# Kernel tuning notes

Hardware: AMD Instinct MI355X
Metric: run time of the kernel (lower is better)

The kernel has to match this reference:

```python
import jax, jax.numpy as jnp
import numpy as np

V = 100000
E = 1600000
IN_CH = 128
HEADS = 4
OUT_CH = 16
NEG_SLOPE = 0.2


def setup_inputs() -> dict:
    key = jax.random.key(0)
    k1, k2, k3, k4, k5 = jax.random.split(key, 5)
    x = jax.random.normal(k1, (V, IN_CH), dtype=jnp.float32)
    edge_index = jax.random.randint(k2, (2, E), 0, V, dtype=jnp.int32)
    # Xavier-ish scaled params
    W = jax.random.normal(k3, (IN_CH, HEADS * OUT_CH), dtype=jnp.float32) / np.sqrt(IN_CH)
    a_src = jax.random.normal(k4, (HEADS, OUT_CH), dtype=jnp.float32) / np.sqrt(OUT_CH)
    a_dst = jax.random.normal(k5, (HEADS, OUT_CH), dtype=jnp.float32) / np.sqrt(OUT_CH)
    return {"x": x, "edge_index": edge_index, "W": W, "a_src": a_src, "a_dst": a_dst}


def reference(x, edge_index, W, a_src, a_dst):
    v = x.shape[0]
    h, cout = a_src.shape
    z = (x @ W).reshape(v, h, cout)                      # [V,H,C]
    src, dst = edge_index[0], edge_index[1]
    # per-node attention logits, then gather at edges (same math as gather-then-dot)
    e_src = jnp.einsum("vhc,hc->vh", z, a_src)           # [V,H]
    e_dst = jnp.einsum("vhc,hc->vh", z, a_dst)           # [V,H]
    e = jax.nn.leaky_relu(e_src[src] + e_dst[dst], NEG_SLOPE)  # [E,H]
    # scatter softmax over dst per head
    m = jax.ops.segment_max(e, dst, num_segments=v)      # [V,H]
    # nodes with no incoming edges get -inf max; edges never reference them
    exp_e = jnp.exp(e - m[dst])                          # [E,H]
    denom = jax.ops.segment_sum(exp_e, dst, num_segments=v)  # [V,H]
    alpha = exp_e / (denom[dst] + 1e-9)                  # [E,H]
    # scatter aggregation of weighted source features
    agg = jax.ops.segment_sum(z[src] * alpha[:, :, None], dst, num_segments=v)  # [V,H,C]
    out = jax.nn.elu(agg)
    return out.reshape(v, h * cout)
```

## Files before the change

kernel.cpp:

```cpp
#include <hip/hip_runtime.h>
#include <hip/hip_bf16.h>
#include <cstdint>

#define NV 100000
#define NE 1600000
#define KIN 128
#define NH 4
#define NC 16
#define NF 64
#define NBKT 391
#define BCAP 4608
#define EPW 16
#define BINWG 391
#define GEMMWG 1563
#define XSTR 136

typedef __attribute__((ext_vector_type(8))) short bf16x8;
typedef __attribute__((ext_vector_type(4))) float f32x4;

__device__ __forceinline__ short f2bf(float f) {
    unsigned u = __float_as_uint(f);
    return (short)((u + 0x7FFFu + ((u >> 16) & 1u)) >> 16);
}

__global__ __launch_bounds__(256) void k_prep(
    const float* __restrict__ W, short* __restrict__ wfrag)
{
    const int t = threadIdx.x;
#pragma unroll
    for (int it = 0; it < 4; ++it) {
        const int idx = it * 256 + t;
        const int lane = idx & 63;
        const int ctks = idx >> 6;
        const int ct = ctks >> 2, ks = ctks & 3;
        const int n = lane & 15, quad = lane >> 4;
        short* dst = wfrag + (size_t)idx * 8;
#pragma unroll
        for (int j = 0; j < 8; ++j) {
            const int k = ks * 32 + quad * 8 + j;
            dst[j] = f2bf(W[k * NF + ct * 16 + n]);
        }
    }
}

__global__ __launch_bounds__(256) void k_front(
    const float* __restrict__ x, const short* __restrict__ wfrag,
    const float* __restrict__ a_src, const float* __restrict__ a_dst,
    __hip_bfloat16* __restrict__ z, float* __restrict__ esrc,
    float* __restrict__ edst,
    const int* __restrict__ ei, int* __restrict__ gcur,
    unsigned* __restrict__ barr)
{
    if (blockIdx.x < BINWG) {
        __shared__ int hist[NBKT];
        __shared__ int base[NBKT];
        const int t = threadIdx.x;
        const int e0 = blockIdx.x * (256 * EPW);

        for (int i = t; i < NBKT; i += 256) hist[i] = 0;
        __syncthreads();

        unsigned pk[EPW];
        short bk[EPW];
#pragma unroll
        for (int i = 0; i < EPW; ++i) {
            const int e = e0 + i * 256 + t;
            if (e < NE) {
                const int s = ei[e];
                const int d = ei[NE + e];
                const int b = d >> 8;
                bk[i] = (short)b;
                pk[i] = ((unsigned)(d & 255) << 17) | (unsigned)s;
                atomicAdd(&hist[b], 1);
            } else {
                bk[i] = -1;
            }
        }
        __syncthreads();
        for (int i = t; i < NBKT; i += 256) {
            const int c = hist[i];
            base[i] = c ? atomicAdd(&gcur[i], c) : 0;
            hist[i] = 0;
        }
        __syncthreads();
#pragma unroll
        for (int i = 0; i < EPW; ++i) {
            if (bk[i] >= 0) {
                const int b = bk[i];
                const int pos = base[b] + atomicAdd(&hist[b], 1);
                barr[(size_t)b * BCAP + pos] = pk[i];
            }
        }
    } else {
        __shared__ short xs[64 * XSTR];
        const int t = threadIdx.x;
        const int bb = blockIdx.x - BINWG;
        const float4* __restrict__ x4 = (const float4*)x;

#pragma unroll
        for (int i = 0; i < 8; ++i) {
            const int li = i * 256 + t;
            const int idx = bb * 2048 + li;
            float4 v = make_float4(0.f, 0.f, 0.f, 0.f);
            if (idx < NV * (KIN / 4)) v = x4[idx];
            short* p = &xs[(li >> 5) * XSTR + (li & 31) * 4];
            p[0] = f2bf(v.x); p[1] = f2bf(v.y);
            p[2] = f2bf(v.z); p[3] = f2bf(v.w);
        }
        __syncthreads();

        const int wv = t >> 6;
        const int lane = t & 63;
        const int n = lane & 15;
        const int quad = lane >> 4;

        bf16x8 bf[16];
        const bf16x8* __restrict__ wf = (const bf16x8*)wfrag;
#pragma unroll
        for (int i = 0; i < 16; ++i) bf[i] = wf[i * 64 + lane];

        const short* __restrict__ arow = &xs[(wv * 16 + n) * XSTR];
        f32x4 acc[4];
#pragma unroll
        for (int ct = 0; ct < 4; ++ct) acc[ct] = (f32x4){0.f, 0.f, 0.f, 0.f};

#pragma unroll
        for (int ks = 0; ks < 4; ++ks) {
            const bf16x8 af = *(const bf16x8*)(arow + ks * 32 + quad * 8);
#pragma unroll
            for (int ct = 0; ct < 4; ++ct)
                acc[ct] = __builtin_amdgcn_mfma_f32_16x16x32_bf16(
                    af, bf[ct * 4 + ks], acc[ct], 0, 0, 0);
        }

        float as[4], ad[4];
#pragma unroll
        for (int ct = 0; ct < 4; ++ct) {
            as[ct] = a_src[ct * 16 + n];
            ad[ct] = a_dst[ct * 16 + n];
        }
        unsigned short* __restrict__ zz = (unsigned short*)z;
#pragma unroll
        for (int ct = 0; ct < 4; ++ct) {
#pragma unroll
            for (int reg = 0; reg < 4; ++reg) {
                const int r_g = bb * 64 + wv * 16 + quad * 4 + reg;
                const float v = acc[ct][reg];
                float ps = v * as[ct];
                float pd = v * ad[ct];
#pragma unroll
                for (int m = 8; m >= 1; m >>= 1) {
                    ps += __shfl_xor(ps, m, 16);
                    pd += __shfl_xor(pd, m, 16);
                }
                if (r_g < NV) {
                    zz[(size_t)r_g * NF + ct * 16 + n] = (unsigned short)f2bf(v);
                    if (n == 0) {
                        esrc[r_g * NH + ct] = ps;
                        edst[r_g * NH + ct] = pd;
                    }
                }
            }
        }
    }
}

__global__ __launch_bounds__(512) void k_csr(
    const int* __restrict__ gcur, unsigned* __restrict__ barr,
    int* __restrict__ row, int* __restrict__ deg)
{
    __shared__ unsigned arr[BCAP];
    __shared__ int hist[256];
    __shared__ int off[256];
    const int t = threadIdx.x;
    const int b = blockIdx.x;
    const int f = gcur[b];
    unsigned* __restrict__ bp = barr + (size_t)b * BCAP;

    for (int i = t; i < f; i += 512) arr[i] = bp[i];
    if (t < 256) hist[t] = 0;
    __syncthreads();
    for (int i = t; i < f; i += 512) atomicAdd(&hist[arr[i] >> 17], 1);
    __syncthreads();
    if (t < 256) off[t] = hist[t];
    __syncthreads();
    for (int s = 1; s < 256; s <<= 1) {
        const int v = (t < 256 && t >= s) ? off[t - s] : 0;
        __syncthreads();
        if (t < 256) off[t] += v;
        __syncthreads();
    }
    if (t < 256) {
        const int excl = off[t] - hist[t];
        const int d = b * 256 + t;
        if (d < NV) {
            row[d] = b * BCAP + excl;
            deg[d] = hist[t];
        }
        off[t] = excl;
        hist[t] = 0;
    }
    __syncthreads();
    for (int i = t; i < f; i += 512) {
        const unsigned p = arr[i];
        const int dl = p >> 17;
        const int slot = off[dl] + atomicAdd(&hist[dl], 1);
        bp[slot] = p & 0x1FFFFu;
    }
}

__global__ __launch_bounds__(256) void k_agg(
    const int* __restrict__ row, const int* __restrict__ deg,
    const unsigned* __restrict__ col,
    const float* __restrict__ esrc, const float* __restrict__ edst,
    const __hip_bfloat16* __restrict__ z, float* __restrict__ out)
{
    __shared__ unsigned lsw[4][64][8];
    const int wv = threadIdx.x >> 6;
    const int lane = threadIdx.x & 63;
    const int quad = lane >> 4;
    const int li = lane & 15;
    const int h = li >> 2;
    const int d = (blockIdx.x * 256 + threadIdx.x) >> 6;
    const int begin = row[d];
    const int nd = deg[d];
    const float4 edv = *(const float4*)(edst + d * 4);
    const unsigned short* __restrict__ z16 = (const unsigned short*)z;

    float a0 = 0.f, a1 = 0.f, a2 = 0.f, a3 = 0.f, den = 0.f;
    for (int base = 0; base < nd; base += 64) {
        const int n = min(64, nd - base);
        unsigned sL = 0;
        float4 w4 = make_float4(0.f, 0.f, 0.f, 0.f);
        if (lane < n) {
            sL = col[begin + base + lane];
            const float4 e4 = *(const float4*)(esrc + sL * 4);
            float ev;
            ev = e4.x + edv.x; ev = ev > 0.f ? ev : 0.2f * ev; w4.x = __expf(ev);
            ev = e4.y + edv.y; ev = ev > 0.f ? ev : 0.2f * ev; w4.y = __expf(ev);
            ev = e4.z + edv.z; ev = ev > 0.f ? ev : 0.2f * ev; w4.z = __expf(ev);
            ev = e4.w + edv.w; ev = ev > 0.f ? ev : 0.2f * ev; w4.w = __expf(ev);
        }
        uint4 st0, st1;
        st0.x = sL; st0.y = __float_as_uint(w4.x);
        st0.z = sL; st0.w = __float_as_uint(w4.y);
        st1.x = sL; st1.y = __float_as_uint(w4.z);
        st1.z = sL; st1.w = __float_as_uint(w4.w);
        *(uint4*)&lsw[wv][lane][0] = st0;
        *(uint4*)&lsw[wv][lane][4] = st1;
#pragma unroll 4
        for (int j = 0; j < n; j += 4) {
            const uint2 sw = *(const uint2*)&lsw[wv][j + quad][h * 2];
            const float w = __uint_as_float(sw.y);
            const uint2 zv = *(const uint2*)(z16 + (((size_t)sw.x << 4) + li) * 4);
            a0 = fmaf(w, __uint_as_float(zv.x << 16), a0);
            a1 = fmaf(w, __uint_as_float(zv.x & 0xFFFF0000u), a1);
            a2 = fmaf(w, __uint_as_float(zv.y << 16), a2);
            a3 = fmaf(w, __uint_as_float(zv.y & 0xFFFF0000u), a3);
            den += w;
        }
    }
    a0 += __shfl_xor(a0, 16); a0 += __shfl_xor(a0, 32);
    a1 += __shfl_xor(a1, 16); a1 += __shfl_xor(a1, 32);
    a2 += __shfl_xor(a2, 16); a2 += __shfl_xor(a2, 32);
    a3 += __shfl_xor(a3, 16); a3 += __shfl_xor(a3, 32);
    den += __shfl_xor(den, 16); den += __shfl_xor(den, 32);
    if (lane < 16) {
        const float id = 1.f / (den + 1e-9f);
        float v0 = a0 * id, v1 = a1 * id, v2 = a2 * id, v3 = a3 * id;
        v0 = v0 > 0.f ? v0 : expm1f(v0);
        v1 = v1 > 0.f ? v1 : expm1f(v1);
        v2 = v2 > 0.f ? v2 : expm1f(v2);
        v3 = v3 > 0.f ? v3 : expm1f(v3);
        *(float4*)(out + (size_t)d * NF + li * 4) = make_float4(v0, v1, v2, v3);
    }
}

extern "C" void kernel_launch(void* const* d_in, const int* in_sizes, int n_in,
                              void* d_out, int out_size, void* d_ws, size_t ws_size,
                              hipStream_t stream)
{
    const float* x     = (const float*)d_in[0];
    const int*   ei    = (const int*)d_in[1];
    const float* W     = (const float*)d_in[2];
    const float* a_src = (const float*)d_in[3];
    const float* a_dst = (const float*)d_in[4];
    float* out = (float*)d_out;

    char* p = (char*)d_ws;
    __hip_bfloat16* z = (__hip_bfloat16*)p;  p += (size_t)NV * NF * 2;
    float* esrc = (float*)p;                 p += (size_t)NV * NH * 4;
    float* edst = (float*)p;                 p += (size_t)NV * NH * 4;
    int*   row  = (int*)p;                   p += (size_t)NV * 4;
    int*   deg  = (int*)p;                   p += (size_t)NV * 4;
    int*   gcur = (int*)p;                   p += (size_t)NBKT * 4;
    p = (char*)(((uintptr_t)p + 255) & ~(uintptr_t)255);
    short* wfrag = (short*)p;                p += (size_t)1024 * 8 * 2;
    p = (char*)(((uintptr_t)p + 255) & ~(uintptr_t)255);
    unsigned* barr = (unsigned*)p;           p += (size_t)NBKT * BCAP * 4;

    hipMemsetAsync(gcur, 0, (size_t)NBKT * 4, stream);

    k_prep<<<1, 256, 0, stream>>>(W, wfrag);
    k_front<<<BINWG + GEMMWG, 256, 0, stream>>>(x, wfrag, a_src, a_dst, z,
                                                esrc, edst, ei, gcur, barr);
    k_csr<<<NBKT, 512, 0, stream>>>(gcur, barr, row, deg);
    k_agg<<<(NV * 64) / 256, 256, 0, stream>>>(row, deg, barr, esrc, edst, z, out);
}
```

Measured before the change: 196.1 us.

## Precompute quantized edge weights in CSR pass, pack into 64-bit records

Moves the per-edge leaky-relu/exp attention weight computation from the aggregation kernel into the CSR build kernel, quantizing each head's weight to an 11-bit exponent-mantissa code packed with the source index into a 64-bit record. The aggregation kernel then reads one record per edge instead of gathering esrc and edst, which shrinks its shared staging. The memset is folded into k_prep and ELU uses __expf-1 instead of expm1f. The 11-bit weight encoding with clamping loses precision and range, which may affect accuracy, and the CSR kernel now does the random esrc gathers.

Result: faster. 188.6 us (-3.8%).

```diff
diff --git a/kernel.cpp b/kernel.cpp
--- a/kernel.cpp
+++ b/kernel.cpp
@@ -23,10 +23,18 @@
     return (short)((u + 0x7FFFu + ((u >> 16) & 1u)) >> 16);
 }
 
+__device__ __forceinline__ unsigned enc11(float w) {
+    unsigned t = (__float_as_uint(w) + 0x10000u) >> 17;
+    t = min(max(t, 7168u), 9215u);
+    return t - 7168u;
+}
+
 __global__ __launch_bounds__(256) void k_prep(
-    const float* __restrict__ W, short* __restrict__ wfrag)
+    const float* __restrict__ W, short* __restrict__ wfrag,
+    int* __restrict__ gcur)
 {
     const int t = threadIdx.x;
+    for (int i = t; i < NBKT; i += 256) gcur[i] = 0;
 #pragma unroll
     for (int it = 0; it < 4; ++it) {
         const int idx = it * 256 + t;
@@ -49,13 +57,14 @@
     __hip_bfloat16* __restrict__ z, float* __restrict__ esrc,
     float* __restrict__ edst,
     const int* __restrict__ ei, int* __restrict__ gcur,
-    unsigned* __restrict__ barr)
+    unsigned long long* __restrict__ barr)
 {
     if (blockIdx.x < BINWG) {
         __shared__ int hist[NBKT];
         __shared__ int base[NBKT];
         const int t = threadIdx.x;
         const int e0 = blockIdx.x * (256 * EPW);
+        unsigned* __restrict__ b32 = (unsigned*)barr;
 
         for (int i = t; i < NBKT; i += 256) hist[i] = 0;
         __syncthreads();
@@ -88,7 +97,7 @@
             if (bk[i] >= 0) {
                 const int b = bk[i];
                 const int pos = base[b] + atomicAdd(&hist[b], 1);
-                barr[(size_t)b * BCAP + pos] = pk[i];
+                b32[(size_t)b * (BCAP * 2) + pos] = pk[i];
             }
         }
     } else {
@@ -166,19 +175,27 @@
 }
 
 __global__ __launch_bounds__(512) void k_csr(
-    const int* __restrict__ gcur, unsigned* __restrict__ barr,
-    int* __restrict__ row, int* __restrict__ deg)
+    const int* __restrict__ gcur, unsigned long long* __restrict__ barr,
+    int* __restrict__ row, int* __restrict__ deg,
+    const float* __restrict__ esrc, const float* __restrict__ edst)
 {
     __shared__ unsigned arr[BCAP];
     __shared__ int hist[256];
     __shared__ int off[256];
+    __shared__ float4 led[256];
     const int t = threadIdx.x;
     const int b = blockIdx.x;
     const int f = gcur[b];
-    unsigned* __restrict__ bp = barr + (size_t)b * BCAP;
-
-    for (int i = t; i < f; i += 512) arr[i] = bp[i];
-    if (t < 256) hist[t] = 0;
+    unsigned* __restrict__ bp32 = (unsigned*)(barr + (size_t)b * BCAP);
+    unsigned long long* __restrict__ bp64 = barr + (size_t)b * BCAP;
+
+    for (int i = t; i < f; i += 512) arr[i] = bp32[i];
+    if (t < 256) {
+        hist[t] = 0;
+        const int d = b * 256 + t;
+        led[t] = (d < NV) ? *(const float4*)(edst + (size_t)d * 4)
+                          : make_float4(0.f, 0.f, 0.f, 0.f);
+    }
     __syncthreads();
     for (int i = t; i < f; i += 512) atomicAdd(&hist[arr[i] >> 17], 1);
     __syncthreads();
@@ -204,55 +221,57 @@
     for (int i = t; i < f; i += 512) {
         const unsigned p = arr[i];
         const int dl = p >> 17;
+        const unsigned s = p & 0x1FFFFu;
         const int slot = off[dl] + atomicAdd(&hist[dl], 1);
-        bp[slot] = p & 0x1FFFFu;
+        const float4 e4 = *(const float4*)(esrc + (size_t)s * 4);
+        const float4 ed = led[dl];
+        float ev;
+        ev = e4.x + ed.x; ev = ev > 0.f ? ev : 0.2f * ev;
+        const unsigned w0 = enc11(__expf(ev));
+        ev = e4.y + ed.y; ev = ev > 0.f ? ev : 0.2f * ev;
+        const unsigned w1 = enc11(__expf(ev));
+        ev = e4.z + ed.z; ev = ev > 0.f ? ev : 0.2f * ev;
+        const unsigned w2 = enc11(__expf(ev));
+        ev = e4.w + ed.w; ev = ev > 0.f ? ev : 0.2f * ev;
+        const unsigned w3 = enc11(__expf(ev));
+        unsigned long long rec = s
+            | ((unsigned long long)w0 << 17)
+            | ((unsigned long long)w1 << 28)
+            | ((unsigned long long)w2 << 39)
+            | ((unsigned long long)w3 << 50);
+        bp64[slot] = rec;
     }
 }
 
 __global__ __launch_bounds__(256) void k_agg(
     const int* __restrict__ row, const int* __restrict__ deg,
-    const unsigned* __restrict__ col,
-    const float* __restrict__ esrc, const float* __restrict__ edst,
+    const unsigned long long* __restrict__ recs,
     const __hip_bfloat16* __restrict__ z, float* __restrict__ out)
 {
-    __shared__ unsigned lsw[4][64][8];
+    __shared__ unsigned long long lsw[4][64];
     const int wv = threadIdx.x >> 6;
     const int lane = threadIdx.x & 63;
     const int quad = lane >> 4;
     const int li = lane & 15;
-    const int h = li >> 2;
+    const int sh = 17 + 11 * (li >> 2);
     const int d = (blockIdx.x * 256 + threadIdx.x) >> 6;
     const int begin = row[d];
     const int nd = deg[d];
-    const float4 edv = *(const float4*)(edst + d * 4);
     const unsigned short* __restrict__ z16 = (const unsigned short*)z;
 
     float a0 = 0.f, a1 = 0.f, a2 = 0.f, a3 = 0.f, den = 0.f;
     for (int base = 0; base < nd; base += 64) {
         const int n = min(64, nd - base);
-        unsigned sL = 0;
-        float4 w4 = make_float4(0.f, 0.f, 0.f, 0.f);
-        if (lane < n) {
-            sL = col[begin + base + lane];
-            const float4 e4 = *(const float4*)(esrc + sL * 4);
-            float ev;
-            ev = e4.x + edv.x; ev = ev > 0.f ? ev : 0.2f * ev; w4.x = __expf(ev);
-            ev = e4.y + edv.y; ev = ev > 0.f ? ev : 0.2f * ev; w4.y = __expf(ev);
-            ev = e4.z + edv.z; ev = ev > 0.f ? ev : 0.2f * ev; w4.z = __expf(ev);
-            ev = e4.w + edv.w; ev = ev > 0.f ? ev : 0.2f * ev; w4.w = __expf(ev);
-        }
-        uint4 st0, st1;
-        st0.x = sL; st0.y = __float_as_uint(w4.x);
-        st0.z = sL; st0.w = __float_as_uint(w4.y);
-        st1.x = sL; st1.y = __float_as_uint(w4.z);
-        st1.z = sL; st1.w = __float_as_uint(w4.w);
-        *(uint4*)&lsw[wv][lane][0] = st0;
-        *(uint4*)&lsw[wv][lane][4] = st1;
+        const unsigned long long rec =
+            (lane < n) ? recs[(size_t)begin + base + lane] : 0ull;
+        lsw[wv][lane] = rec;
 #pragma unroll 4
         for (int j = 0; j < n; j += 4) {
-            const uint2 sw = *(const uint2*)&lsw[wv][j + quad][h * 2];
-            const float w = __uint_as_float(sw.y);
-            const uint2 zv = *(const uint2*)(z16 + (((size_t)sw.x << 4) + li) * 4);
+            const unsigned long long r = lsw[wv][j + quad];
+            const unsigned s = (unsigned)r & 0x1FFFFu;
+            const unsigned wu = ((unsigned)(r >> sh)) & 0x7FFu;
+            const float w = __uint_as_float((wu + 7168u) << 17);
+            const uint2 zv = *(const uint2*)(z16 + ((size_t)s << 6) + li * 4);
             a0 = fmaf(w, __uint_as_float(zv.x << 16), a0);
             a1 = fmaf(w, __uint_as_float(zv.x & 0xFFFF0000u), a1);
             a2 = fmaf(w, __uint_as_float(zv.y << 16), a2);
@@ -268,10 +287,10 @@
     if (lane < 16) {
         const float id = 1.f / (den + 1e-9f);
         float v0 = a0 * id, v1 = a1 * id, v2 = a2 * id, v3 = a3 * id;
-        v0 = v0 > 0.f ? v0 : expm1f(v0);
-        v1 = v1 > 0.f ? v1 : expm1f(v1);
-        v2 = v2 > 0.f ? v2 : expm1f(v2);
-        v3 = v3 > 0.f ? v3 : expm1f(v3);
+        v0 = v0 > 0.f ? v0 : __expf(v0) - 1.f;
+        v1 = v1 > 0.f ? v1 : __expf(v1) - 1.f;
+        v2 = v2 > 0.f ? v2 : __expf(v2) - 1.f;
+        v3 = v3 > 0.f ? v3 : __expf(v3) - 1.f;
         *(float4*)(out + (size_t)d * NF + li * 4) = make_float4(v0, v1, v2, v3);
     }
 }
@@ -297,13 +316,12 @@
     p = (char*)(((uintptr_t)p + 255) & ~(uintptr_t)255);
     short* wfrag = (short*)p;                p += (size_t)1024 * 8 * 2;
     p = (char*)(((uintptr_t)p + 255) & ~(uintptr_t)255);
-    unsigned* barr = (unsigned*)p;           p += (size_t)NBKT * BCAP * 4;
-
-    hipMemsetAsync(gcur, 0, (size_t)NBKT * 4, stream);
-
-    k_prep<<<1, 256, 0, stream>>>(W, wfrag);
+    unsigned long long* barr = (unsigned long long*)p;
+    p += (size_t)NBKT * BCAP * 8;
+
+    k_prep<<<1, 256, 0, stream>>>(W, wfrag, gcur);
     k_front<<<BINWG + GEMMWG, 256, 0, stream>>>(x, wfrag, a_src, a_dst, z,
                                                 esrc, edst, ei, gcur, barr);
-    k_csr<<<NBKT, 512, 0, stream>>>(gcur, barr, row, deg);
-    k_agg<<<(NV * 64) / 256, 256, 0, stream>>>(row, deg, barr, esrc, edst, z, out);
-}
+    k_csr<<<NBKT, 512, 0, stream>>>(gcur, barr, row, deg, esrc, edst);
+    k_agg<<<(NV * 64) / 256, 256, 0, stream>>>(row, deg, barr, z, out);
+}
```
